# Kernel optimization log

Hardware: AMD Instinct MI355X
Metric: run time of the kernel (lower is better)

## Reference

```python
import jax, jax.numpy as jnp
from jax import lax
import numpy as np

B, T, F, V, L, H, E = 64, 512, 161, 32, 64, 128, 32
CONV_IN = 1152  # 32 channels * 36 freq after the two convs


def setup_inputs() -> dict:
    key = jax.random.key(0)
    ks = jax.random.split(key, 16)
    g = lambda k, s, sc=0.05: jax.random.normal(k, s, dtype=jnp.float32) * sc
    return {
        "x": jax.random.normal(ks[0], (B, T, F), dtype=jnp.float32),
        "y": jax.random.randint(ks[1], (B, L), 0, V),
        "mean": jnp.zeros((F,), jnp.float32),
        "std": jnp.ones((F,), jnp.float32),
        "conv1_w": g(ks[2], (32, 1, 32, 2)),
        "conv1_b": jnp.zeros((32,), jnp.float32),
        "conv2_w": g(ks[3], (32, 32, 32, 9), 0.02),
        "conv2_b": jnp.zeros((32,), jnp.float32),
        "gru_w_ih": g(ks[4], (3 * H, CONV_IN)),
        "gru_w_hh": g(ks[5], (3 * H, H)),
        "gru_b_ih": jnp.zeros((3 * H,), jnp.float32),
        "gru_b_hh": jnp.zeros((3 * H,), jnp.float32),
        "emb": g(ks[6], (V, E), 0.1),
        "dec_w_ih": g(ks[7], (3 * H, E)),
        "dec_w_hh": g(ks[8], (3 * H, H)),
        "dec_b_ih": jnp.zeros((3 * H,), jnp.float32),
        "dec_b_hh": jnp.zeros((3 * H,), jnp.float32),
        "fc_w": g(ks[9], (V, H)),
        "fc_b": jnp.zeros((V,), jnp.float32),
    }


def _gru_step(h, xp, w_hh, b_hh):
    # torch GRU/GRUCell gate math
    gh = h @ w_hh.T + b_hh
    xr, xz, xn = jnp.split(xp, 3, axis=-1)
    hr, hz, hn = jnp.split(gh, 3, axis=-1)
    r = jax.nn.sigmoid(xr + hr)
    z = jax.nn.sigmoid(xz + hz)
    n = jnp.tanh(xn + r * hn)
    return (1.0 - z) * n + z * h


def _forward(x, y, mean, std, conv1_w, conv1_b, conv2_w, conv2_b,
             gru_w_ih, gru_w_hh, gru_b_ih, gru_b_hh, emb,
             dec_w_ih, dec_w_hh, dec_b_ih, dec_b_hh, fc_w, fc_b):
    dn = ("NCHW", "OIHW", "NCHW")
    x = (x - mean) / std                       # (B,T,F)
    x = x[:, None]                             # (B,1,T,F)
    x = jax.nn.relu(lax.conv_general_dilated(x, conv1_w, (2, 2), "VALID", dimension_numbers=dn) + conv1_b[None, :, None, None])
    x = jax.nn.relu(lax.conv_general_dilated(x, conv2_w, (2, 2), "VALID", dimension_numbers=dn) + conv2_b[None, :, None, None])
    x = x.transpose(0, 2, 1, 3)                # (B,t,C,F') like torch transpose(1,2)
    b, t, c, f = x.shape
    x = x.reshape(b, t, c * f)                 # (B,t,1152)

    # encoder GRU via scan; precompute input projections for all timesteps
    xp = x @ gru_w_ih.T + gru_b_ih             # (B,t,3H)
    h0 = jnp.zeros((b, gru_w_hh.shape[1]), x.dtype)
    def enc_step(h, xpt):
        h = _gru_step(h, xpt, gru_w_hh, gru_b_hh)
        return h, h
    _, hs = lax.scan(enc_step, h0, xp.transpose(1, 0, 2))
    eh = hs.transpose(1, 0, 2)                 # (B,t,H)

    # decode_train: GRUCell + bmm-softmax attention per label step
    emb_in = emb[y[:, :-1]]                    # (B,L-1,E)
    ip = emb_in @ dec_w_ih.T + dec_b_ih        # (B,L-1,3H)
    hx0 = jnp.zeros((b, dec_w_hh.shape[1]), x.dtype)
    def dec_step(hx, ipt):
        hx2 = _gru_step(hx, ipt, dec_w_hh, dec_b_hh)
        s = jnp.einsum("btd,bd->bt", eh, hx2)  # bmm scores
        a = jax.nn.softmax(s, axis=-1)
        ctx = jnp.einsum("btd,bt->bd", eh, a)  # attention context replaces hx
        return ctx, ctx
    _, ctxs = lax.scan(dec_step, hx0, ip.transpose(1, 0, 2))
    out = ctxs.transpose(1, 0, 2) @ fc_w.T + fc_b  # (B,L-1,V)
    return out


def reference(x, y, mean, std, conv1_w, conv1_b, conv2_w, conv2_b,
              gru_w_ih, gru_w_hh, gru_b_ih, gru_b_hh, emb,
              dec_w_ih, dec_w_hh, dec_b_ih, dec_b_hh, fc_w, fc_b):
    return _forward(x, y, mean, std, conv1_w, conv1_b, conv2_w, conv2_b,
                    gru_w_ih, gru_w_hh, gru_b_ih, gru_b_hh, emb,
                    dec_w_ih, dec_w_hh, dec_b_ih, dec_b_hh, fc_w, fc_b)
```

## Files before the change

### kernel.cpp

```cpp
#include <hip/hip_runtime.h>


typedef float f32x4 __attribute__((ext_vector_type(4)));
typedef short s16x8 __attribute__((ext_vector_type(8)));

static __device__ __forceinline__ unsigned short f2b(float f) {
  unsigned int u = __float_as_uint(f);
  unsigned int r = u + 0x7fffu + ((u >> 16) & 1u);
  return (unsigned short)(r >> 16);
}
static __device__ __forceinline__ float sigmoidf_(float x) {
  return 1.0f / (1.0f + __expf(-x));
}
static __device__ __forceinline__ float tanhf_(float x) {
  float ax = fabsf(x);
  float t = __expf(-2.0f * ax);
  float r = (1.0f - t) / (1.0f + t);
  return x >= 0.0f ? r : -r;
}
static __device__ __forceinline__ float blo(unsigned int w) {
  return __uint_as_float(w << 16);
}
static __device__ __forceinline__ float bhi(unsigned int w) {
  return __uint_as_float(w & 0xffff0000u);
}
static __device__ __forceinline__ void barL() {
  asm volatile("s_waitcnt lgkmcnt(0)" ::: "memory");
  __builtin_amdgcn_s_barrier();
  asm volatile("" ::: "memory");
}

__global__ __launch_bounds__(256) void prep_kernel(
    const float* __restrict__ w2, const float* __restrict__ wih,
    const float* __restrict__ whh, const float* __restrict__ dwhh,
    const float* __restrict__ dwih,
    unsigned short* __restrict__ wt2, unsigned short* __restrict__ wihB,
    unsigned int* __restrict__ wpe, unsigned int* __restrict__ wpd,
    float* __restrict__ wdT) {
  int idx = blockIdx.x * 256 + threadIdx.x;
  if (idx < 294912) {
    int ci = idx & 31;
    int n = (idx >> 5) & 31;
    int kk = idx >> 10;
    int kf = kk % 9, kt = kk / 9;
    wt2[idx] = f2b(w2[((n * 32 + ci) * 32 + kt) * 9 + kf]);
  } else if (idx < 737280) {
    int i = idx - 294912;
    wihB[i] = f2b(wih[i]);
  } else if (idx < 761856) {
    int i = idx - 737280;
    int j = i % 384, k2 = i / 384;
    unsigned int lo = f2b(whh[j * 128 + 2 * k2]);
    unsigned int hi = f2b(whh[j * 128 + 2 * k2 + 1]);
    wpe[i] = lo | (hi << 16);
  } else if (idx < 786432) {
    int i = idx - 761856;
    int j = i % 384, k2 = i / 384;
    unsigned int lo = f2b(dwhh[j * 128 + 2 * k2]);
    unsigned int hi = f2b(dwhh[j * 128 + 2 * k2 + 1]);
    wpd[i] = lo | (hi << 16);
  } else if (idx < 798720) {
    int i = idx - 786432;
    int j = i % 384, e = i / 384;
    wdT[i] = dwih[j * 32 + e];
  }
}

__global__ __launch_bounds__(256) void conv1_kernel(
    const float* __restrict__ x, const float* __restrict__ mean,
    const float* __restrict__ stdv, const float* __restrict__ w1,
    const float* __restrict__ b1, unsigned short* __restrict__ c1out) {
  __shared__ float ins[46][162];
  __shared__ float meanL[161];
  __shared__ float rstdL[161];
  int tid = threadIdx.x;
  int tt = blockIdx.x;
  int b = blockIdx.y;
  int t0 = tt * 8;
  if (tid < 161) {
    meanL[tid] = mean[tid];
    rstdL[tid] = 1.0f / stdv[tid];
  }
  int c = tid & 31, fs = tid >> 5;
  float w[64];
  {
    const float4* wp = (const float4*)(w1 + c * 64);
#pragma unroll
    for (int i = 0; i < 16; ++i) {
      float4 v = wp[i];
      w[4 * i] = v.x; w[4 * i + 1] = v.y; w[4 * i + 2] = v.z; w[4 * i + 3] = v.w;
    }
  }
  float bias = b1[c];
  __syncthreads();

  const float* xb = x + ((size_t)b * 512 + 2 * t0) * 161;
  int nrows = 512 - 2 * t0; if (nrows > 46) nrows = 46;
  for (int i = tid; i < 46 * 161; i += 256) {
    int r = i / 161, col = i - r * 161;
    float v = (r < nrows) ? xb[(size_t)r * 161 + col] : 0.0f;
    ins[r][col] = (v - meanL[col]) * rstdL[col];
  }
  __syncthreads();

  int T = 241 - t0; if (T > 8) T = 8;
#pragma unroll
  for (int fi = 0; fi < 10; ++fi) {
    int f = fs + 8 * fi;
    float acc[8];
#pragma unroll
    for (int t = 0; t < 8; ++t) acc[t] = bias;
#pragma unroll
    for (int r = 0; r < 46; ++r) {
      float2 v = *(const float2*)&ins[r][2 * f];
#pragma unroll
      for (int t = 0; t < 8; ++t) {
        const int kt = r - 2 * t;
        if (kt >= 0 && kt < 32) {
          acc[t] = fmaf(v.x, w[2 * kt], acc[t]);
          acc[t] = fmaf(v.y, w[2 * kt + 1], acc[t]);
        }
      }
    }
#pragma unroll
    for (int t = 0; t < 8; ++t) {
      if (t < T) {
        float a = acc[t] > 0.0f ? acc[t] : 0.0f;
        unsigned int h = (unsigned int)f2b(a);
        unsigned int o = __shfl_xor(h, 1);
        if (!(c & 1)) {
          unsigned int pk = h | (o << 16);
          *(unsigned int*)&c1out[(((size_t)b * 241 + t0 + t) * 80 + f) * 32 + c] = pk;
        }
      }
    }
  }
}

__global__ __launch_bounds__(256) void conv2_kernel(
    const unsigned short* __restrict__ c1out, const unsigned short* __restrict__ wt2,
    const float* __restrict__ b2, unsigned short* __restrict__ X2) {
  __shared__ __align__(16) int ldsA[8 * 360 * 4];
  __shared__ __align__(16) int ldsB[4608];
  int tid = threadIdx.x;
  int lane = tid & 63, wave = tid >> 6;
  int quad = lane >> 4, l16 = lane & 15;
  int j = blockIdx.x;
  int b = blockIdx.y;

  int tlA[4], baseA[4];
#pragma unroll
  for (int mt = 0; mt < 4; ++mt) {
    int ml = wave * 64 + mt * 16 + l16;
    if (ml > 251) ml = 251;
    int tl = ml / 36;
    int f2 = ml - tl * 36;
    tlA[mt] = tl;
    baseA[mt] = (9 * f2 + quad) * 4;
  }

  f32x4 zero = {0.f, 0.f, 0.f, 0.f};
  f32x4 acc[4][2];
#pragma unroll
  for (int mt = 0; mt < 4; ++mt) {
    acc[mt][0] = zero;
    acc[mt][1] = zero;
  }

  const size_t rowsh = 2560;
  const unsigned short* gbase = c1out + ((size_t)b * 241 + 14 * j) * rowsh;
  int ra = tid;
  int rb = (tid < 64) ? 256 + tid : 319;
  int bc4 = (tid < 128) ? 1024 + tid : 1151;
  const unsigned short* bkl = (const unsigned short*)ldsB + l16 * 32 + quad * 8;

  for (int p = 0; p < 2; ++p) {
#pragma unroll
    for (int k = 0; k < 9; ++k) {
      int i = tid + 256 * k;
      if (i < 2240) {
        int h = i / 320, r = i - 320 * h;
        int4 v = *(const int4*)(gbase + (size_t)(p + 2 * h) * rowsh + r * 8);
        *((int4*)&ldsA[(h * 360 + r + (r >> 3)) * 4]) = v;
      }
    }
    {
      const int4* bs = (const int4*)(wt2 + (size_t)p * 9216);
#pragma unroll
      for (int i = 0; i < 4; ++i) {
        int4 v = bs[tid + 256 * i];
        *((int4*)&ldsB[(tid + 256 * i) * 4]) = v;
      }
      if (tid < 128) {
        int4 v = bs[1024 + tid];
        *((int4*)&ldsB[(1024 + tid) * 4]) = v;
      }
    }
    asm volatile("" ::: "memory");
    const unsigned short* g7 = gbase + (size_t)(p + 14) * rowsh;
    int4 La = *(const int4*)(g7 + ra * 8);
    int4 Lb = *(const int4*)(g7 + rb * 8);
    const int4* bsn = (const int4*)(wt2 + (size_t)(p + 2) * 9216);
    int4 Bv0 = bsn[tid];
    int4 Bv1 = bsn[tid + 256];
    int4 Bv2 = bsn[tid + 512];
    int4 Bv3 = bsn[tid + 768];
    int4 Bv4 = bsn[bc4];
    asm volatile("" ::: "memory");
    barL();

    for (int k = 0; k < 16; ++k) {
#pragma unroll
      for (int kf = 0; kf < 9; ++kf) {
        s16x8 b0 = *(const s16x8*)(bkl + kf * 1024);
        s16x8 b1v = *(const s16x8*)(bkl + kf * 1024 + 512);
        int kfo = (4 * kf + (kf >> 1)) * 4;
#pragma unroll
        for (int mt = 0; mt < 4; ++mt) {
          int slot = (k + tlA[mt]) & 7;
          s16x8 a = *(const s16x8*)&ldsA[slot * 1440 + baseA[mt] + kfo];
          acc[mt][0] = __builtin_amdgcn_mfma_f32_16x16x32_bf16(a, b0, acc[mt][0], 0, 0, 0);
          acc[mt][1] = __builtin_amdgcn_mfma_f32_16x16x32_bf16(a, b1v, acc[mt][1], 0, 0, 0);
        }
      }
      barL();
      if (k < 15) {
        asm volatile("s_waitcnt vmcnt(0)" ::: "memory");
        int slot = (k + 7) & 7;
        *((int4*)&ldsA[(slot * 360 + ra + (ra >> 3)) * 4]) = La;
        if (tid < 64) *((int4*)&ldsA[(slot * 360 + rb + (rb >> 3)) * 4]) = Lb;
        *((int4*)&ldsB[tid * 4]) = Bv0;
        *((int4*)&ldsB[(tid + 256) * 4]) = Bv1;
        *((int4*)&ldsB[(tid + 512) * 4]) = Bv2;
        *((int4*)&ldsB[(tid + 768) * 4]) = Bv3;
        if (tid < 128) *((int4*)&ldsB[(1024 + tid) * 4]) = Bv4;
        if (k <= 13) {
          const unsigned short* gn = gbase + (size_t)(p + 2 * (k + 8)) * rowsh;
          La = *(const int4*)(gn + ra * 8);
          Lb = *(const int4*)(gn + rb * 8);
          const int4* bs2 = (const int4*)(wt2 + (size_t)(2 * (k + 2) + p) * 9216);
          Bv0 = bs2[tid];
          Bv1 = bs2[tid + 256];
          Bv2 = bs2[tid + 512];
          Bv3 = bs2[tid + 768];
          Bv4 = bs2[bc4];
        }
        asm volatile("" ::: "memory");
        barL();
      }
    }
  }

#pragma unroll
  for (int nt = 0; nt < 2; ++nt) {
    int n = nt * 16 + l16;
    float bias = b2[n];
#pragma unroll
    for (int mt = 0; mt < 4; ++mt) {
      f32x4 v = acc[mt][nt];
#pragma unroll
      for (int r = 0; r < 4; ++r) {
        int ml = wave * 64 + mt * 16 + quad * 4 + r;
        if (ml < 252) {
          int tl = ml / 36;
          int f2 = ml - tl * 36;
          int t2 = 7 * j + tl;
          float val = v[r] + bias;
          val = val > 0.0f ? val : 0.0f;
          X2[((size_t)(b * 105 + t2) * 32 + n) * 36 + f2] = f2b(val);
        }
      }
    }
  }
}

__global__ __launch_bounds__(256) void xp_kernel(
    const unsigned short* __restrict__ X2, const unsigned short* __restrict__ wihB,
    const float* __restrict__ bih, float* __restrict__ xp) {
  int tid = threadIdx.x;
  int lane = tid & 63, wave = tid >> 6;
  int quad = lane >> 4, l16 = lane & 15;
  int m_tile = blockIdx.x * 4 + wave;
  int n0 = blockIdx.y * 128;
  int row = m_tile * 16 + l16;
  const unsigned short* apb = X2 + (size_t)row * 1152 + quad * 8;
  const unsigned short* bpb = wihB + (size_t)(n0 + l16) * 1152 + quad * 8;
  f32x4 zero = {0.f, 0.f, 0.f, 0.f};
  f32x4 acc[8];
#pragma unroll
  for (int nt = 0; nt < 8; ++nt) acc[nt] = zero;
  for (int ks = 0; ks < 36; ++ks) {
    s16x8 a = *(const s16x8*)(apb + ks * 32);
#pragma unroll
    for (int nt = 0; nt < 8; ++nt) {
      s16x8 bb = *(const s16x8*)(bpb + (size_t)nt * 16 * 1152 + ks * 32);
      acc[nt] = __builtin_amdgcn_mfma_f32_16x16x32_bf16(a, bb, acc[nt], 0, 0, 0);
    }
  }
#pragma unroll
  for (int nt = 0; nt < 8; ++nt) {
    int n = n0 + nt * 16 + l16;
    float bias = bih[n];
#pragma unroll
    for (int r = 0; r < 4; ++r) {
      int m = m_tile * 16 + quad * 4 + r;
      xp[(size_t)m * 384 + n] = acc[nt][r] + bias;
    }
  }
}

__global__ __launch_bounds__(384) void ip_kernel(
    const int* __restrict__ y, const float* __restrict__ emb,
    const float* __restrict__ wdT, const float* __restrict__ dbih,
    float* __restrict__ ipg) {
  __shared__ float er[32];
  int bs = blockIdx.x;
  int b = bs / 63, s = bs - b * 63;
  int tid = threadIdx.x;
  if (tid < 32) er[tid] = emb[(size_t)y[b * 64 + s] * 32 + tid];
  __syncthreads();
  float acc = dbih[tid];
#pragma unroll
  for (int e = 0; e < 32; ++e) acc = fmaf(er[e], wdT[e * 384 + tid], acc);
  ipg[(size_t)bs * 384 + tid] = acc;
}

__global__ __launch_bounds__(384) void rnn_kernel(
    const float* __restrict__ xp, const unsigned int* __restrict__ wpe,
    const float* __restrict__ bhh, const float* __restrict__ ipg,
    const unsigned int* __restrict__ wpd, const float* __restrict__ dbhh,
    const float* __restrict__ fcw, const float* __restrict__ fcb,
    float* __restrict__ outg) {
  __shared__ __align__(16) float ehT[128 * 116];
  __shared__ __align__(16) float ehR[105 * 132];
  __shared__ __align__(16) float gh_s[384];
  __shared__ __align__(16) float h_s[128];
  __shared__ __align__(16) float hx2_s[128];
  __shared__ __align__(16) float a_s[112];
  __shared__ float red_s[1];
  int tid = threadIdx.x, b = blockIdx.x;

  f32x4 wq[32];
#pragma unroll
  for (int q = 0; q < 32; ++q) {
    unsigned int w0 = wpe[(2 * q) * 384 + tid];
    unsigned int w1 = wpe[(2 * q + 1) * 384 + tid];
    f32x4 t = {blo(w0), bhi(w0), blo(w1), bhi(w1)};
    wq[q] = t;
  }
  float bias = bhh[tid];
  if (tid < 128) h_s[tid] = 0.0f;
  if (tid < 112) a_s[tid] = 0.0f;
  for (int i = tid; i < 128 * 11; i += 384) {
    int d = i / 11, t = 105 + i - (i / 11) * 11;
    ehT[d * 116 + t] = 0.0f;
  }
  barL();

  const float* xpb = xp + (size_t)b * 105 * 384;
  float nxg = (tid < 256) ? xpb[tid] : 0.0f;
  float nxn = (tid < 128) ? xpb[tid + 256] : 0.0f;
  for (int t = 0; t < 105; ++t) {
    float cxg = nxg, cxn = nxn;
    if (t < 104) {
      const float* xpt = xpb + (size_t)(t + 1) * 384;
      nxg = (tid < 256) ? xpt[tid] : 0.0f;
      nxn = (tid < 128) ? xpt[tid + 256] : 0.0f;
    }
    f32x4 accA = {bias, 0.f, 0.f, 0.f};
    f32x4 accB = {0.f, 0.f, 0.f, 0.f};
#pragma unroll
    for (int q = 0; q < 32; q += 2) {
      f32x4 hA = *(const f32x4*)&h_s[4 * q];
      f32x4 hB = *(const f32x4*)&h_s[4 * q + 4];
      accA = __builtin_elementwise_fma(hA, wq[q], accA);
      accB = __builtin_elementwise_fma(hB, wq[q + 1], accB);
    }
    float acc = ((accA.x + accA.y) + (accA.z + accA.w)) +
                ((accB.x + accB.y) + (accB.z + accB.w));
    gh_s[tid] = (tid < 256) ? sigmoidf_(cxg + acc) : acc;
    barL();
    if (tid < 128) {
      float r = gh_s[tid], z = gh_s[tid + 128], hnp = gh_s[tid + 256];
      float nn = tanhf_(cxn + r * hnp);
      float hn = (1.0f - z) * nn + z * h_s[tid];
      h_s[tid] = hn;
      ehT[tid * 116 + t] = hn;
      ehR[t * 132 + tid] = hn;
    }
    barL();
  }

#pragma unroll
  for (int q = 0; q < 32; ++q) {
    unsigned int w0 = wpd[(2 * q) * 384 + tid];
    unsigned int w1 = wpd[(2 * q + 1) * 384 + tid];
    f32x4 t = {blo(w0), bhi(w0), blo(w1), bhi(w1)};
    wq[q] = t;
  }
  bias = dbhh[tid];
  f32x4 wf4[8];
  float fcbv = 0.0f;
  int fv = 0, fp = 0;
  if (tid >= 256) {
    int i = tid - 256;
    fp = i & 3; fv = i >> 2;
#pragma unroll
    for (int d = 0; d < 8; ++d) wf4[d] = *(const f32x4*)&fcw[fv * 128 + fp * 32 + 4 * d];
    fcbv = fcb[fv];
  }
  if (tid < 128) h_s[tid] = 0.0f;
  if (tid == 0) red_s[0] = 1.0f;
  barL();

  const float* ipb = ipg + (size_t)b * 63 * 384;
  nxg = (tid < 256) ? ipb[tid] : 0.0f;
  nxn = (tid < 128) ? ipb[tid + 256] : 0.0f;
  for (int s = 0; s < 63; ++s) {
    float cxg = nxg, cxn = nxn;
    if (s < 62) {
      const float* ipt = ipb + (size_t)(s + 1) * 384;
      nxg = (tid < 256) ? ipt[tid] : 0.0f;
      nxn = (tid < 128) ? ipt[tid + 256] : 0.0f;
    }
    float rsum = red_s[0];
    f32x4 accA = {0.f, 0.f, 0.f, 0.f};
    f32x4 accB = {0.f, 0.f, 0.f, 0.f};
#pragma unroll
    for (int q = 0; q < 32; q += 2) {
      f32x4 hA = *(const f32x4*)&h_s[4 * q];
      f32x4 hB = *(const f32x4*)&h_s[4 * q + 4];
      accA = __builtin_elementwise_fma(hA, wq[q], accA);
      accB = __builtin_elementwise_fma(hB, wq[q + 1], accB);
    }
    float dot = ((accA.x + accA.y) + (accA.z + accA.w)) +
                ((accB.x + accB.y) + (accB.z + accB.w));
    float acc = fmaf(rsum, dot, bias);
    gh_s[tid] = (tid < 256) ? sigmoidf_(cxg + acc) : acc;
    barL();
    if (tid < 128) {
      float r = gh_s[tid], z = gh_s[tid + 128], hnp = gh_s[tid + 256];
      float nn = tanhf_(cxn + r * hnp);
      hx2_s[tid] = (1.0f - z) * nn + z * (rsum * h_s[tid]);
    }
    barL();

    if (tid < 256) {
      int row = tid >> 1; if (row > 104) row = 104;
      int part = tid & 1;
      const float* erow = &ehR[row * 132 + part * 64];
      const float* hp = &hx2_s[part * 64];
      f32x4 sv = {0.f, 0.f, 0.f, 0.f};
#pragma unroll
      for (int jj = 0; jj < 16; ++jj) {
        f32x4 e4 = *(const f32x4*)&erow[4 * jj];
        f32x4 h4 = *(const f32x4*)&hp[4 * jj];
        sv = __builtin_elementwise_fma(e4, h4, sv);
      }
      float sc = (sv.x + sv.y) + (sv.z + sv.w);
      sc += __shfl_xor(sc, 1);
      if (part == 0 && tid < 210) a_s[row] = __expf(fminf(sc, 75.0f));
    } else if (s > 0) {
      const f32x4* cx = (const f32x4*)&h_s[fp * 32];
      f32x4 pv = {0.f, 0.f, 0.f, 0.f};
#pragma unroll
      for (int d = 0; d < 8; ++d) pv = __builtin_elementwise_fma(cx[d], wf4[d], pv);
      float p = (pv.x + pv.z) + (pv.y + pv.w);
      p += __shfl_xor(p, 1);
      p += __shfl_xor(p, 2);
      if (fp == 0) outg[((size_t)b * 63 + (s - 1)) * 32 + fv] = fmaf(p, rsum, fcbv);
    }
    barL();

    if (tid < 256) {
      int d = tid >> 1, half = tid & 1;
      const float* erow = &ehT[d * 116 + half * 56];
      const float* ap = &a_s[half * 56];
      f32x4 cv = {0.f, 0.f, 0.f, 0.f};
#pragma unroll
      for (int jj = 0; jj < 14; ++jj) {
        f32x4 e4 = *(const f32x4*)&erow[4 * jj];
        f32x4 a4 = *(const f32x4*)&ap[4 * jj];
        cv = __builtin_elementwise_fma(e4, a4, cv);
      }
      float c = (cv.x + cv.y) + (cv.z + cv.w);
      c += __shfl_xor(c, 1);
      if (half == 0) h_s[d] = c;
    } else if (tid < 320) {
      int l = tid - 256;
      float sv = a_s[l] + ((l < 48) ? a_s[64 + l] : 0.0f);
      sv += __shfl_xor(sv, 1);
      sv += __shfl_xor(sv, 2);
      sv += __shfl_xor(sv, 4);
      sv += __shfl_xor(sv, 8);
      sv += __shfl_xor(sv, 16);
      sv += __shfl_xor(sv, 32);
      if (l == 0) red_s[0] = 1.0f / sv;
    }
    barL();
  }

  if (tid >= 256) {
    float rs = red_s[0];
    const f32x4* cx = (const f32x4*)&h_s[fp * 32];
    f32x4 pv = {0.f, 0.f, 0.f, 0.f};
#pragma unroll
    for (int d = 0; d < 8; ++d) pv = __builtin_elementwise_fma(cx[d], wf4[d], pv);
    float p = (pv.x + pv.z) + (pv.y + pv.w);
    p += __shfl_xor(p, 1);
    p += __shfl_xor(p, 2);
    if (fp == 0) outg[((size_t)b * 63 + 62) * 32 + fv] = fmaf(p, rs, fcbv);
  }
}

extern "C" void kernel_launch(void* const* d_in, const int* in_sizes, int n_in,
                              void* d_out, int out_size, void* d_ws, size_t ws_size,
                              hipStream_t stream) {
  const float* x = (const float*)d_in[0];
  const int* y = (const int*)d_in[1];
  const float* mean = (const float*)d_in[2];
  const float* stdv = (const float*)d_in[3];
  const float* w1 = (const float*)d_in[4];
  const float* b1 = (const float*)d_in[5];
  const float* w2 = (const float*)d_in[6];
  const float* b2 = (const float*)d_in[7];
  const float* wih = (const float*)d_in[8];
  const float* whh = (const float*)d_in[9];
  const float* bih = (const float*)d_in[10];
  const float* bhh = (const float*)d_in[11];
  const float* emb = (const float*)d_in[12];
  const float* dwih = (const float*)d_in[13];
  const float* dwhh = (const float*)d_in[14];
  const float* dbih = (const float*)d_in[15];
  const float* dbhh = (const float*)d_in[16];
  const float* fcw = (const float*)d_in[17];
  const float* fcb = (const float*)d_in[18];
  float* out = (float*)d_out;
  char* ws = (char*)d_ws;

  unsigned short* c1out = (unsigned short*)(ws + 0);
  float* xp = (float*)(ws + 0);
  float* ipg = (float*)(ws + 13762560);
  unsigned short* wt2 = (unsigned short*)(ws + 78970880);
  unsigned short* wihB = (unsigned short*)(ws + 79560704);
  unsigned int* wpe = (unsigned int*)(ws + 80445440);
  unsigned int* wpd = (unsigned int*)(ws + 80543744);
  float* wdT = (float*)(ws + 80642048);
  unsigned short* X2 = (unsigned short*)(ws + 80691200);

  prep_kernel<<<3120, 256, 0, stream>>>(w2, wih, whh, dwhh, dwih, wt2, wihB, wpe, wpd, wdT);
  conv1_kernel<<<dim3(31, 64), 256, 0, stream>>>(x, mean, stdv, w1, b1, c1out);
  conv2_kernel<<<dim3(15, 64), 256, 0, stream>>>(c1out, wt2, b2, X2);
  xp_kernel<<<dim3(105, 3), 256, 0, stream>>>(X2, wihB, bih, xp);
  ip_kernel<<<64 * 63, 384, 0, stream>>>(y, emb, wdT, dbih, ipg);
  rnn_kernel<<<64, 384, 0, stream>>>(xp, wpe, bhh, ipg, wpd, dbhh, fcw, fcb, out);
}
```

Baseline: 649.5 us.

## Compute all three encoder GRU gates per thread to drop one barrier per step

The encoder recurrence now has only threads 0-127 do the work, each holding packed bf16 weights for all three gates (192 registers) and computing r, z and n itself. The gh_s shared-memory exchange and one block barrier per timestep go away, and the hidden state is carried in a register. In exchange, two thirds of the threads sit idle during the encoder, each active thread does three times the FMA work, and register pressure from 192 packed weight words risks spills or lower occupancy.

```diff
diff --git a/kernel.cpp b/kernel.cpp
--- a/kernel.cpp
+++ b/kernel.cpp
@@ -340,57 +340,97 @@
   __shared__ float red_s[1];
   int tid = threadIdx.x, b = blockIdx.x;
 
+  {
+    unsigned int wp0[64], wp1[64], wp2[64];
+    float bi0 = 0.0f, bi1 = 0.0f, bi2 = 0.0f;
+    if (tid < 128) {
+#pragma unroll
+      for (int k2 = 0; k2 < 64; ++k2) {
+        wp0[k2] = wpe[k2 * 384 + tid];
+        wp1[k2] = wpe[k2 * 384 + tid + 128];
+        wp2[k2] = wpe[k2 * 384 + tid + 256];
+      }
+      bi0 = bhh[tid];
+      bi1 = bhh[tid + 128];
+      bi2 = bhh[tid + 256];
+    }
+    if (tid < 128) h_s[tid] = 0.0f;
+    if (tid < 112) a_s[tid] = 0.0f;
+    for (int i = tid; i < 128 * 11; i += 384) {
+      int d = i / 11, t = 105 + i - (i / 11) * 11;
+      ehT[d * 116 + t] = 0.0f;
+    }
+    barL();
+
+    const float* xpb = xp + (size_t)b * 105 * 384;
+    float hreg = 0.0f;
+    float nx0 = 0.f, nx1 = 0.f, nx2 = 0.f;
+    if (tid < 128) {
+      nx0 = xpb[tid];
+      nx1 = xpb[tid + 128];
+      nx2 = xpb[tid + 256];
+    }
+    for (int t = 0; t < 105; ++t) {
+      if (tid < 128) {
+        float cx0 = nx0, cx1 = nx1, cx2 = nx2;
+        if (t < 104) {
+          const float* xpt = xpb + (size_t)(t + 1) * 384;
+          nx0 = xpt[tid];
+          nx1 = xpt[tid + 128];
+          nx2 = xpt[tid + 256];
+        }
+        f32x4 aA0 = {bi0, 0.f, 0.f, 0.f}, aB0 = {0.f, 0.f, 0.f, 0.f};
+        f32x4 aA1 = {bi1, 0.f, 0.f, 0.f}, aB1 = {0.f, 0.f, 0.f, 0.f};
+        f32x4 aA2 = {bi2, 0.f, 0.f, 0.f}, aB2 = {0.f, 0.f, 0.f, 0.f};
+#pragma unroll
+        for (int q = 0; q < 32; q += 2) {
+          f32x4 hA = *(const f32x4*)&h_s[4 * q];
+          f32x4 hB = *(const f32x4*)&h_s[4 * q + 4];
+          {
+            unsigned int a0 = wp0[2 * q], a1 = wp0[2 * q + 1];
+            unsigned int b0 = wp0[2 * q + 2], b1 = wp0[2 * q + 3];
+            f32x4 wA = {blo(a0), bhi(a0), blo(a1), bhi(a1)};
+            f32x4 wB = {blo(b0), bhi(b0), blo(b1), bhi(b1)};
+            aA0 = __builtin_elementwise_fma(hA, wA, aA0);
+            aB0 = __builtin_elementwise_fma(hB, wB, aB0);
+          }
+          {
+            unsigned int a0 = wp1[2 * q], a1 = wp1[2 * q + 1];
+            unsigned int b0 = wp1[2 * q + 2], b1 = wp1[2 * q + 3];
+            f32x4 wA = {blo(a0), bhi(a0), blo(a1), bhi(a1)};
+            f32x4 wB = {blo(b0), bhi(b0), blo(b1), bhi(b1)};
+            aA1 = __builtin_elementwise_fma(hA, wA, aA1);
+            aB1 = __builtin_elementwise_fma(hB, wB, aB1);
+          }
+          {
+            unsigned int a0 = wp2[2 * q], a1 = wp2[2 * q + 1];
+            unsigned int b0 = wp2[2 * q + 2], b1 = wp2[2 * q + 3];
+            f32x4 wA = {blo(a0), bhi(a0), blo(a1), bhi(a1)};
+            f32x4 wB = {blo(b0), bhi(b0), blo(b1), bhi(b1)};
+            aA2 = __builtin_elementwise_fma(hA, wA, aA2);
+            aB2 = __builtin_elementwise_fma(hB, wB, aB2);
+          }
+        }
+        float acc0 = ((aA0.x + aA0.y) + (aA0.z + aA0.w)) +
+                     ((aB0.x + aB0.y) + (aB0.z + aB0.w));
+        float acc1 = ((aA1.x + aA1.y) + (aA1.z + aA1.w)) +
+                     ((aB1.x + aB1.y) + (aB1.z + aB1.w));
+        float acc2 = ((aA2.x + aA2.y) + (aA2.z + aA2.w)) +
+                     ((aB2.x + aB2.y) + (aB2.z + aB2.w));
+        float r = sigmoidf_(cx0 + acc0);
+        float z = sigmoidf_(cx1 + acc1);
+        float nn = tanhf_(cx2 + r * acc2);
+        float hn = (1.0f - z) * nn + z * hreg;
+        hreg = hn;
+        h_s[tid] = hn;
+        ehT[tid * 116 + t] = hn;
+        ehR[t * 132 + tid] = hn;
+      }
+      barL();
+    }
+  }
+
   f32x4 wq[32];
-#pragma unroll
-  for (int q = 0; q < 32; ++q) {
-    unsigned int w0 = wpe[(2 * q) * 384 + tid];
-    unsigned int w1 = wpe[(2 * q + 1) * 384 + tid];
-    f32x4 t = {blo(w0), bhi(w0), blo(w1), bhi(w1)};
-    wq[q] = t;
-  }
-  float bias = bhh[tid];
-  if (tid < 128) h_s[tid] = 0.0f;
-  if (tid < 112) a_s[tid] = 0.0f;
-  for (int i = tid; i < 128 * 11; i += 384) {
-    int d = i / 11, t = 105 + i - (i / 11) * 11;
-    ehT[d * 116 + t] = 0.0f;
-  }
-  barL();
-
-  const float* xpb = xp + (size_t)b * 105 * 384;
-  float nxg = (tid < 256) ? xpb[tid] : 0.0f;
-  float nxn = (tid < 128) ? xpb[tid + 256] : 0.0f;
-  for (int t = 0; t < 105; ++t) {
-    float cxg = nxg, cxn = nxn;
-    if (t < 104) {
-      const float* xpt = xpb + (size_t)(t + 1) * 384;
-      nxg = (tid < 256) ? xpt[tid] : 0.0f;
-      nxn = (tid < 128) ? xpt[tid + 256] : 0.0f;
-    }
-    f32x4 accA = {bias, 0.f, 0.f, 0.f};
-    f32x4 accB = {0.f, 0.f, 0.f, 0.f};
-#pragma unroll
-    for (int q = 0; q < 32; q += 2) {
-      f32x4 hA = *(const f32x4*)&h_s[4 * q];
-      f32x4 hB = *(const f32x4*)&h_s[4 * q + 4];
-      accA = __builtin_elementwise_fma(hA, wq[q], accA);
-      accB = __builtin_elementwise_fma(hB, wq[q + 1], accB);
-    }
-    float acc = ((accA.x + accA.y) + (accA.z + accA.w)) +
-                ((accB.x + accB.y) + (accB.z + accB.w));
-    gh_s[tid] = (tid < 256) ? sigmoidf_(cxg + acc) : acc;
-    barL();
-    if (tid < 128) {
-      float r = gh_s[tid], z = gh_s[tid + 128], hnp = gh_s[tid + 256];
-      float nn = tanhf_(cxn + r * hnp);
-      float hn = (1.0f - z) * nn + z * h_s[tid];
-      h_s[tid] = hn;
-      ehT[tid * 116 + t] = hn;
-      ehR[t * 132 + tid] = hn;
-    }
-    barL();
-  }
-
 #pragma unroll
   for (int q = 0; q < 32; ++q) {
     unsigned int w0 = wpd[(2 * q) * 384 + tid];
@@ -398,7 +438,7 @@
     f32x4 t = {blo(w0), bhi(w0), blo(w1), bhi(w1)};
     wq[q] = t;
   }
-  bias = dbhh[tid];
+  float bias = dbhh[tid];
   f32x4 wf4[8];
   float fcbv = 0.0f;
   int fv = 0, fp = 0;
@@ -414,8 +454,8 @@
   barL();
 
   const float* ipb = ipg + (size_t)b * 63 * 384;
-  nxg = (tid < 256) ? ipb[tid] : 0.0f;
-  nxn = (tid < 128) ? ipb[tid + 256] : 0.0f;
+  float nxg = (tid < 256) ? ipb[tid] : 0.0f;
+  float nxn = (tid < 128) ? ipb[tid + 256] : 0.0f;
   for (int s = 0; s < 63; ++s) {
     float cxg = nxg, cxn = nxn;
     if (s < 62) {
```

New measurement: 1.526 ms. 135% more time.
